# Performance work log

Measured on AMD Instinct MI355X. Metric: run time of the kernel, lower is better.

Reference implementation:

```python
import jax, jax.numpy as jnp
import numpy as np

DIM = 1024
N_HEADS = 16
HEAD_DIM = DIM // N_HEADS


def setup_inputs() -> dict:
    key = jax.random.key(0)
    ks = jax.random.split(key, 5)
    scale = 1.0 / np.sqrt(DIM)
    x = jax.random.normal(ks[0], (2, 2048, DIM), dtype=jnp.float32)
    W_qkv = jax.random.normal(ks[1], (DIM, 3 * DIM), dtype=jnp.float32) * scale
    b_qkv = jax.random.normal(ks[2], (3 * DIM,), dtype=jnp.float32) * 0.01
    W_proj = jax.random.normal(ks[3], (DIM, DIM), dtype=jnp.float32) * scale
    b_proj = jax.random.normal(ks[4], (DIM,), dtype=jnp.float32) * 0.01
    return {"x": x, "W_qkv": W_qkv, "b_qkv": b_qkv, "W_proj": W_proj, "b_proj": b_proj}


def reference(x, W_qkv, b_qkv, W_proj, b_proj):
    B, T, C = x.shape
    qkv = x @ W_qkv + b_qkv  # [B,T,3C]
    q, k, v = jnp.split(qkv, 3, axis=2)
    # [B,T,C] -> [B,H,T,Dh]
    def heads(y):
        return y.reshape(B, T, N_HEADS, HEAD_DIM).transpose(0, 2, 1, 3)
    q, k, v = heads(q), heads(k), heads(v)
    inv_sqrt_dh = 1.0 / jnp.sqrt(jnp.asarray(HEAD_DIM, dtype=x.dtype))
    attn = jnp.einsum('bhqd,bhkd->bhqk', q, k) * inv_sqrt_dh
    attn = jax.nn.softmax(attn, axis=-1)
    out = jnp.einsum('bhqk,bhkd->bhqd', attn, v)
    out = out.transpose(0, 2, 1, 3).reshape(B, T, C)
    return out @ W_proj + b_proj
```

## Files before the change

### kernel.cpp

```cpp
#include <hip/hip_runtime.h>
#include <hip/hip_bf16.h>
#include <math.h>

using bf16 = __hip_bfloat16;

typedef __bf16 bf16x8 __attribute__((ext_vector_type(8)));
typedef __bf16 bf16x4 __attribute__((ext_vector_type(4)));
typedef float  f32x4  __attribute__((ext_vector_type(4)));

constexpr int Bb = 2;
constexpr int Ts = 2048;
constexpr int Cc = 1024;
constexpr int Hh = 16;
constexpr int Dh = 64;
constexpr int Mm = Bb * Ts;
constexpr int Nqkv = 3 * Cc;
constexpr int BHTD = Bb * Hh * Ts * Dh;

__device__ __forceinline__
void gll16(const __bf16* g, __bf16* l)
{
    __builtin_amdgcn_global_load_lds(
        (const __attribute__((address_space(1))) unsigned int*)g,
        (__attribute__((address_space(3))) unsigned int*)l,
        16, 0, 0);
}

__global__ __launch_bounds__(256)
void cvt_bf16(const float* __restrict__ in, __bf16* __restrict__ out)
{
    int i = (blockIdx.x * 256 + threadIdx.x) * 4;
    float4 v = *(const float4*)(in + i);
    bf16x4 o = { (__bf16)v.x, (__bf16)v.y, (__bf16)v.z, (__bf16)v.w };
    *(bf16x4*)(out + i) = o;
}

__global__ __launch_bounds__(256)
void cvt_transpose(const float* __restrict__ W, __bf16* __restrict__ Wt, int cols)
{
    __shared__ __bf16 tl[64][72];
    const int t  = threadIdx.x;
    const int c0 = blockIdx.x * 64;
    const int r0 = blockIdx.y * 64;
    #pragma unroll
    for (int i = 0; i < 4; i++) {
        int e = t + 256 * i;
        int r = e >> 4, c4 = (e & 15) * 4;
        float4 v = *(const float4*)(W + (r0 + r) * cols + c0 + c4);
        bf16x4 o = { (__bf16)v.x, (__bf16)v.y, (__bf16)v.z, (__bf16)v.w };
        *(bf16x4*)&tl[r][c4] = o;
    }
    __syncthreads();
    #pragma unroll
    for (int i = 0; i < 4; i++) {
        int e = t + 256 * i;
        int n = e >> 4, k4 = (e & 15) * 4;
        bf16x4 o = { tl[k4][n], tl[k4 + 1][n], tl[k4 + 2][n], tl[k4 + 3][n] };
        *(bf16x4*)(Wt + (c0 + n) * 1024 + r0 + k4) = o;
    }
}

__device__ __forceinline__
void gemm_core(const __bf16* __restrict__ A, const __bf16* __restrict__ Bt,
               int m0, int n0, int wm, int wn, int quad, int l16, int t,
               f32x4 (&acc)[4][4])
{
    __shared__ __bf16 Al[128][32];
    __shared__ __bf16 Bl[128][32];

    const int wave = t >> 6;
    const int lane = t & 63;
    const int srow = lane >> 2;
    const int scol = (lane & 3) * 8;

    const __bf16* Ag = A  + (size_t)(m0 + wave * 16 + srow) * 1024 + scol;
    const __bf16* Bg = Bt + (size_t)(n0 + wave * 16 + srow) * 1024 + scol;
    __bf16* Al_lo = &Al[wave * 16][0];
    __bf16* Al_hi = &Al[64 + wave * 16][0];
    __bf16* Bl_lo = &Bl[wave * 16][0];
    __bf16* Bl_hi = &Bl[64 + wave * 16][0];

    for (int k0 = 0; k0 < 1024; k0 += 32) {
        gll16(Ag + k0,             Al_lo);
        gll16(Ag + k0 + 64 * 1024, Al_hi);
        gll16(Bg + k0,             Bl_lo);
        gll16(Bg + k0 + 64 * 1024, Bl_hi);
        __syncthreads();
        bf16x8 af[4], bfr[4];
        #pragma unroll
        for (int mt = 0; mt < 4; mt++)
            af[mt] = *(const bf16x8*)&Al[wm * 64 + mt * 16 + l16][quad * 8];
        #pragma unroll
        for (int nt = 0; nt < 4; nt++)
            bfr[nt] = *(const bf16x8*)&Bl[wn * 64 + nt * 16 + l16][quad * 8];
        #pragma unroll
        for (int mt = 0; mt < 4; mt++)
            #pragma unroll
            for (int nt = 0; nt < 4; nt++)
                acc[mt][nt] = __builtin_amdgcn_mfma_f32_16x16x32_bf16(
                    af[mt], bfr[nt], acc[mt][nt], 0, 0, 0);
        __syncthreads();
    }
}

__global__ __launch_bounds__(256)
void qkv_mfma(const __bf16* __restrict__ A, const __bf16* __restrict__ Bt,
              const float* __restrict__ bias, __bf16* __restrict__ qkv)
{
    const int t    = threadIdx.x;
    const int wave = t >> 6;
    const int lane = t & 63;
    const int quad = lane >> 4;
    const int l16  = lane & 15;
    const int wm   = wave >> 1, wn = wave & 1;
    const int n0 = blockIdx.x * 128;
    const int m0 = blockIdx.y * 128;

    f32x4 acc[4][4];
    #pragma unroll
    for (int i = 0; i < 4; i++)
        #pragma unroll
        for (int j = 0; j < 4; j++)
            acc[i][j] = f32x4{0.f, 0.f, 0.f, 0.f};

    gemm_core(A, Bt, m0, n0, wm, wn, quad, l16, t, acc);

    #pragma unroll
    for (int nt = 0; nt < 4; nt++) {
        int n = n0 + wn * 64 + nt * 16 + l16;
        float bs = bias[n];
        int which = n >> 10;
        int c = n & 1023;
        int h = c >> 6;
        int d = c & 63;
        if (which == 2) {
            #pragma unroll
            for (int mt = 0; mt < 4; mt++) {
                int m = m0 + wm * 64 + mt * 16 + quad * 4;
                int b = m >> 11;
                int tt = m & 2047;
                bf16x4 o = { (__bf16)(acc[mt][nt][0] + bs),
                             (__bf16)(acc[mt][nt][1] + bs),
                             (__bf16)(acc[mt][nt][2] + bs),
                             (__bf16)(acc[mt][nt][3] + bs) };
                *(bf16x4*)&qkv[2 * (size_t)BHTD +
                               (((size_t)(b * 16 + h) * 64 + d) * 2048 + tt)] = o;
            }
        } else {
            #pragma unroll
            for (int mt = 0; mt < 4; mt++) {
                #pragma unroll
                for (int r = 0; r < 4; r++) {
                    int m = m0 + wm * 64 + mt * 16 + quad * 4 + r;
                    int b = m >> 11;
                    int tt = m & 2047;
                    qkv[which * (size_t)BHTD +
                        (((b * 16 + h) * 2048 + tt) * 64 + d)] =
                        (__bf16)(acc[mt][nt][r] + bs);
                }
            }
        }
    }
}

__global__ __launch_bounds__(256)
void proj_mfma(const __bf16* __restrict__ A, const __bf16* __restrict__ Bt,
               const float* __restrict__ bias, float* __restrict__ out)
{
    const int t    = threadIdx.x;
    const int wave = t >> 6;
    const int lane = t & 63;
    const int quad = lane >> 4;
    const int l16  = lane & 15;
    const int wm   = wave >> 1, wn = wave & 1;
    const int n0 = blockIdx.x * 128;
    const int m0 = blockIdx.y * 128;

    f32x4 acc[4][4];
    #pragma unroll
    for (int i = 0; i < 4; i++)
        #pragma unroll
        for (int j = 0; j < 4; j++)
            acc[i][j] = f32x4{0.f, 0.f, 0.f, 0.f};

    gemm_core(A, Bt, m0, n0, wm, wn, quad, l16, t, acc);

    #pragma unroll
    for (int nt = 0; nt < 4; nt++) {
        int n = n0 + wn * 64 + nt * 16 + l16;
        float bs = bias[n];
        #pragma unroll
        for (int mt = 0; mt < 4; mt++) {
            #pragma unroll
            for (int r = 0; r < 4; r++) {
                int m = m0 + wm * 64 + mt * 16 + quad * 4 + r;
                out[m * 1024 + n] = acc[mt][nt][r] + bs;
            }
        }
    }
}

__global__ __launch_bounds__(256)
void attn_mfma(const __bf16* __restrict__ Q, const __bf16* __restrict__ K,
               const __bf16* __restrict__ VT, __bf16* __restrict__ O)
{
    __shared__ __bf16 Ks[64][72];
    __shared__ __bf16 Vt[64][72];
    __shared__ __bf16 Pl[4][32][72];

    const int t    = threadIdx.x;
    const int wave = t >> 6;
    const int lane = t & 63;
    const int quad = lane >> 4;
    const int l16  = lane & 15;

    const int blk = blockIdx.x;
    const int bh  = (blk & 7) * 4 + ((blk >> 3) & 3);
    const int qc  = blk >> 5;
    const int q0  = qc * 128 + wave * 32;

    const __bf16* Qp = Q + ((size_t)bh * Ts + q0) * Dh;
    const __bf16* Kp = K + (size_t)bh * Ts * Dh;
    const __bf16* Vp = VT + (size_t)bh * Dh * Ts;

    bf16x8 qf[2][2];
    #pragma unroll
    for (int s = 0; s < 2; s++) {
        qf[s][0] = *(const bf16x8*)(Qp + (s * 16 + l16) * Dh + quad * 8);
        qf[s][1] = *(const bf16x8*)(Qp + (s * 16 + l16) * Dh + quad * 8 + 32);
        #pragma unroll
        for (int i = 0; i < 8; i++) {
            qf[s][0][i] = (__bf16)(0.125f * (float)qf[s][0][i]);
            qf[s][1][i] = (__bf16)(0.125f * (float)qf[s][1][i]);
        }
    }

    const f32x4 zero4 = {0.f, 0.f, 0.f, 0.f};
    f32x4 accO[2][4];
    #pragma unroll
    for (int s = 0; s < 2; s++)
        #pragma unroll
        for (int dt = 0; dt < 4; dt++) accO[s][dt] = zero4;
    float lsum[2] = {0.f, 0.f};

    const int jr = t >> 3;
    const int cc = (t & 7) * 8;
    const __bf16* Kb = Kp + jr * Dh + cc;
    const __bf16* Vb = Vp + jr * Ts + cc;

    bf16x8 ka0 = *(const bf16x8*)(Kb);
    bf16x8 ka1 = *(const bf16x8*)(Kb + 32 * Dh);
    bf16x8 va0 = *(const bf16x8*)(Vb);
    bf16x8 va1 = *(const bf16x8*)(Vb + 32 * Ts);

    for (int ic = 0; ic < Ts / 64; ic++) {
        *(bf16x8*)&Ks[jr][cc]      = ka0;
        *(bf16x8*)&Ks[jr + 32][cc] = ka1;
        *(bf16x8*)&Vt[jr][cc]      = va0;
        *(bf16x8*)&Vt[jr + 32][cc] = va1;
        if (ic < Ts / 64 - 1) {
            int ko = (ic + 1) * 64;
            ka0 = *(const bf16x8*)(Kb + ko * Dh);
            ka1 = *(const bf16x8*)(Kb + ko * Dh + 32 * Dh);
            va0 = *(const bf16x8*)(Vb + ko);
            va1 = *(const bf16x8*)(Vb + ko + 32 * Ts);
        }
        __syncthreads();

        f32x4 st[2][4];
        #pragma unroll
        for (int kt = 0; kt < 4; kt++) {
            bf16x8 k0f = *(const bf16x8*)(&Ks[kt * 16 + l16][quad * 8]);
            bf16x8 k1f = *(const bf16x8*)(&Ks[kt * 16 + l16][quad * 8 + 32]);
            #pragma unroll
            for (int s = 0; s < 2; s++) {
                f32x4 a = zero4;
                a = __builtin_amdgcn_mfma_f32_16x16x32_bf16(k0f, qf[s][0], a, 0, 0, 0);
                a = __builtin_amdgcn_mfma_f32_16x16x32_bf16(k1f, qf[s][1], a, 0, 0, 0);
                st[s][kt] = a;
            }
        }

        #pragma unroll
        for (int s = 0; s < 2; s++) {
            #pragma unroll
            for (int kt = 0; kt < 4; kt++) {
                bf16x4 pb;
                #pragma unroll
                for (int r = 0; r < 4; r++) {
                    float p = __expf(st[s][kt][r]);
                    pb[r] = (__bf16)p;
                    lsum[s] += (float)pb[r];
                }
                *(bf16x4*)&Pl[wave][s * 16 + l16][kt * 16 + quad * 4] = pb;
            }
        }
        bf16x8 pa[2][2];
        #pragma unroll
        for (int s = 0; s < 2; s++) {
            pa[s][0] = *(const bf16x8*)(&Pl[wave][s * 16 + l16][quad * 8]);
            pa[s][1] = *(const bf16x8*)(&Pl[wave][s * 16 + l16][quad * 8 + 32]);
        }

        #pragma unroll
        for (int dt = 0; dt < 4; dt++) {
            bf16x8 vb0 = *(const bf16x8*)(&Vt[l16 + 16 * dt][quad * 8]);
            bf16x8 vb1 = *(const bf16x8*)(&Vt[l16 + 16 * dt][quad * 8 + 32]);
            #pragma unroll
            for (int s = 0; s < 2; s++) {
                accO[s][dt] = __builtin_amdgcn_mfma_f32_16x16x32_bf16(pa[s][0], vb0, accO[s][dt], 0, 0, 0);
                accO[s][dt] = __builtin_amdgcn_mfma_f32_16x16x32_bf16(pa[s][1], vb1, accO[s][dt], 0, 0, 0);
            }
        }
        __syncthreads();
    }

    int b = bh >> 4, h = bh & 15;
    #pragma unroll
    for (int s = 0; s < 2; s++) {
        float l = lsum[s];
        l += __shfl_xor(l, 16);
        l += __shfl_xor(l, 32);
        __bf16* Op = O + ((long)(b * Ts + q0 + s * 16) * Cc) + h * 64;
        #pragma unroll
        for (int r = 0; r < 4; r++) {
            float inv = 1.f / __shfl(l, quad * 4 + r);
            int qrow = quad * 4 + r;
            #pragma unroll
            for (int dt = 0; dt < 4; dt++)
                Op[qrow * Cc + l16 + 16 * dt] = (__bf16)(accO[s][dt][r] * inv);
        }
    }
}

extern "C" void kernel_launch(void* const* d_in, const int* in_sizes, int n_in,
                              void* d_out, int out_size, void* d_ws, size_t ws_size,
                              hipStream_t stream)
{
    (void)in_sizes; (void)n_in; (void)out_size; (void)ws_size;
    const float* x     = (const float*)d_in[0];
    const float* Wqkv  = (const float*)d_in[1];
    const float* bqkv  = (const float*)d_in[2];
    const float* Wproj = (const float*)d_in[3];
    const float* bproj = (const float*)d_in[4];
    float* out = (float*)d_out;

    __bf16* ws   = (__bf16*)d_ws;
    __bf16* Qw   = ws;
    __bf16* XbAO = ws + 3 * (size_t)BHTD;
    __bf16* Wqt  = XbAO + (size_t)Mm * Cc;
    __bf16* Wpt  = Wqt + (size_t)Nqkv * Cc;

    cvt_bf16<<<Mm * Cc / 1024, 256, 0, stream>>>(x, XbAO);
    cvt_transpose<<<dim3(Nqkv / 64, Cc / 64), 256, 0, stream>>>(Wqkv, Wqt, Nqkv);
    cvt_transpose<<<dim3(Cc / 64, Cc / 64), 256, 0, stream>>>(Wproj, Wpt, Cc);
    qkv_mfma<<<dim3(Nqkv / 128, Mm / 128), 256, 0, stream>>>(XbAO, Wqt, bqkv, Qw);
    attn_mfma<<<dim3(512), 256, 0, stream>>>(
        Qw, Qw + BHTD, Qw + 2 * (size_t)BHTD, XbAO);
    proj_mfma<<<dim3(Cc / 128, Mm / 128), 256, 0, stream>>>(XbAO, Wpt, bproj, out);
}
```

Measured before the change: 209.7 us.

## Merge prep kernels, deepen GEMM K-tile to 64, sum unrounded softmax weights

Folds the three conversion and transpose launches into one kernel that dispatches on block index, removing two launch gaps. The shared GEMM core now stages a K-slice of 64 per iteration instead of 32, which halves the barrier and loop count and doubles the MFMAs between syncs, at the cost of twice the LDS per block. The softmax row sum now accumulates the fp32 probability instead of the bf16-rounded one, a small change in both arithmetic and numerics.

```diff
diff --git a/kernel.cpp b/kernel.cpp
--- a/kernel.cpp
+++ b/kernel.cpp
@@ -27,21 +27,31 @@
 }
 
 __global__ __launch_bounds__(256)
-void cvt_bf16(const float* __restrict__ in, __bf16* __restrict__ out)
-{
-    int i = (blockIdx.x * 256 + threadIdx.x) * 4;
-    float4 v = *(const float4*)(in + i);
-    bf16x4 o = { (__bf16)v.x, (__bf16)v.y, (__bf16)v.z, (__bf16)v.w };
-    *(bf16x4*)(out + i) = o;
-}
-
-__global__ __launch_bounds__(256)
-void cvt_transpose(const float* __restrict__ W, __bf16* __restrict__ Wt, int cols)
+void prep_all(const float* __restrict__ x, __bf16* __restrict__ Xb,
+              const float* __restrict__ Wq, __bf16* __restrict__ Wqt,
+              const float* __restrict__ Wp, __bf16* __restrict__ Wpt)
 {
     __shared__ __bf16 tl[64][72];
-    const int t  = threadIdx.x;
-    const int c0 = blockIdx.x * 64;
-    const int r0 = blockIdx.y * 64;
+    const int bid = blockIdx.x;
+    const int t = threadIdx.x;
+
+    if (bid < 4096) {
+        int i = (bid * 256 + t) * 4;
+        float4 v = *(const float4*)(x + i);
+        bf16x4 o = { (__bf16)v.x, (__bf16)v.y, (__bf16)v.z, (__bf16)v.w };
+        *(bf16x4*)(Xb + i) = o;
+        return;
+    }
+    const float* W; __bf16* Wt; int cols, bx, by;
+    if (bid < 4096 + 768) {
+        W = Wq; Wt = Wqt; cols = Nqkv;
+        bx = (bid - 4096) % 48; by = (bid - 4096) / 48;
+    } else {
+        W = Wp; Wt = Wpt; cols = Cc;
+        bx = (bid - 4864) % 16; by = (bid - 4864) / 16;
+    }
+    const int c0 = bx * 64;
+    const int r0 = by * 64;
     #pragma unroll
     for (int i = 0; i < 4; i++) {
         int e = t + 256 * i;
@@ -65,40 +75,43 @@
                int m0, int n0, int wm, int wn, int quad, int l16, int t,
                f32x4 (&acc)[4][4])
 {
-    __shared__ __bf16 Al[128][32];
-    __shared__ __bf16 Bl[128][32];
+    __shared__ __bf16 Al[128 * 64];
+    __shared__ __bf16 Bl[128 * 64];
 
     const int wave = t >> 6;
     const int lane = t & 63;
-    const int srow = lane >> 2;
-    const int scol = (lane & 3) * 8;
-
-    const __bf16* Ag = A  + (size_t)(m0 + wave * 16 + srow) * 1024 + scol;
-    const __bf16* Bg = Bt + (size_t)(n0 + wave * 16 + srow) * 1024 + scol;
-    __bf16* Al_lo = &Al[wave * 16][0];
-    __bf16* Al_hi = &Al[64 + wave * 16][0];
-    __bf16* Bl_lo = &Bl[wave * 16][0];
-    __bf16* Bl_hi = &Bl[64 + wave * 16][0];
-
-    for (int k0 = 0; k0 < 1024; k0 += 32) {
-        gll16(Ag + k0,             Al_lo);
-        gll16(Ag + k0 + 64 * 1024, Al_hi);
-        gll16(Bg + k0,             Bl_lo);
-        gll16(Bg + k0 + 64 * 1024, Bl_hi);
+    const int srow = lane >> 3;
+    const int scol = (lane & 7) * 8;
+
+    const __bf16* Ag = A  + (size_t)(m0 + wave * 32 + srow) * 1024 + scol;
+    const __bf16* Bg = Bt + (size_t)(n0 + wave * 32 + srow) * 1024 + scol;
+
+    for (int k0 = 0; k0 < 1024; k0 += 64) {
+        #pragma unroll
+        for (int c = 0; c < 4; c++) {
+            gll16(Ag + k0 + (size_t)(c * 8) * 1024, Al + (wave * 32 + c * 8) * 64);
+            gll16(Bg + k0 + (size_t)(c * 8) * 1024, Bl + (wave * 32 + c * 8) * 64);
+        }
         __syncthreads();
-        bf16x8 af[4], bfr[4];
+        bf16x8 af[2][4], bfr[2][4];
+        #pragma unroll
+        for (int h = 0; h < 2; h++) {
+            #pragma unroll
+            for (int mt = 0; mt < 4; mt++)
+                af[h][mt] = *(const bf16x8*)&Al[(wm * 64 + mt * 16 + l16) * 64 + h * 32 + quad * 8];
+            #pragma unroll
+            for (int nt = 0; nt < 4; nt++)
+                bfr[h][nt] = *(const bf16x8*)&Bl[(wn * 64 + nt * 16 + l16) * 64 + h * 32 + quad * 8];
+        }
         #pragma unroll
         for (int mt = 0; mt < 4; mt++)
-            af[mt] = *(const bf16x8*)&Al[wm * 64 + mt * 16 + l16][quad * 8];
-        #pragma unroll
-        for (int nt = 0; nt < 4; nt++)
-            bfr[nt] = *(const bf16x8*)&Bl[wn * 64 + nt * 16 + l16][quad * 8];
-        #pragma unroll
-        for (int mt = 0; mt < 4; mt++)
-            #pragma unroll
-            for (int nt = 0; nt < 4; nt++)
+            #pragma unroll
+            for (int nt = 0; nt < 4; nt++) {
                 acc[mt][nt] = __builtin_amdgcn_mfma_f32_16x16x32_bf16(
-                    af[mt], bfr[nt], acc[mt][nt], 0, 0, 0);
+                    af[0][mt], bfr[0][nt], acc[mt][nt], 0, 0, 0);
+                acc[mt][nt] = __builtin_amdgcn_mfma_f32_16x16x32_bf16(
+                    af[1][mt], bfr[1][nt], acc[mt][nt], 0, 0, 0);
+            }
         __syncthreads();
     }
 }
@@ -290,7 +303,7 @@
                 for (int r = 0; r < 4; r++) {
                     float p = __expf(st[s][kt][r]);
                     pb[r] = (__bf16)p;
-                    lsum[s] += (float)pb[r];
+                    lsum[s] += p;
                 }
                 *(bf16x4*)&Pl[wave][s * 16 + l16][kt * 16 + quad * 4] = pb;
             }
@@ -351,9 +364,7 @@
     __bf16* Wqt  = XbAO + (size_t)Mm * Cc;
     __bf16* Wpt  = Wqt + (size_t)Nqkv * Cc;
 
-    cvt_bf16<<<Mm * Cc / 1024, 256, 0, stream>>>(x, XbAO);
-    cvt_transpose<<<dim3(Nqkv / 64, Cc / 64), 256, 0, stream>>>(Wqkv, Wqt, Nqkv);
-    cvt_transpose<<<dim3(Cc / 64, Cc / 64), 256, 0, stream>>>(Wproj, Wpt, Cc);
+    prep_all<<<dim3(5120), 256, 0, stream>>>(x, XbAO, Wqkv, Wqt, Wproj, Wpt);
     qkv_mfma<<<dim3(Nqkv / 128, Mm / 128), 256, 0, stream>>>(XbAO, Wqt, bqkv, Qw);
     attn_mfma<<<dim3(512), 256, 0, stream>>>(
         Qw, Qw + BHTD, Qw + 2 * (size_t)BHTD, XbAO);
```

Result: no change. 209.3 us (-0.2%).
